# Kernel tuning notes

Measured on AMD Instinct MI355X. Metric: run time of the kernel, lower is better.

Reference implementation:

```python
import jax, jax.numpy as jnp
import numpy as np

N_PATCHES = 14
HIDDEN_D = 768
LN_EPS = 1e-5


def positional_embeddings(seq_len, d):
    # sin(i / 10000^(j/d)) for even j, cos(i / 10000^((j-1)/d)) for odd j
    i = jnp.arange(seq_len, dtype=jnp.float32)[:, None]
    j = jnp.arange(d, dtype=jnp.float32)[None, :]
    exponent = (jnp.floor(j / 2.0) * 2.0) / d
    angle = i / jnp.power(10000.0, exponent)
    return jnp.where(jnp.arange(d)[None, :] % 2 == 0, jnp.sin(angle), jnp.cos(angle))


def patchify(images, n_patches):
    # images: [B, C, H, W] -> patches: [B, n_patches^2, C*ph*pw]
    # flatten order per torch patch.flatten(): (C, ph, pw)
    B, C, H, W = images.shape
    ph, pw = H // n_patches, W // n_patches
    x = images.reshape(B, C, n_patches, ph, n_patches, pw)
    x = x.transpose(0, 2, 4, 1, 3, 5)  # [B, ny, nx, C, ph, pw]
    return x.reshape(B, n_patches * n_patches, C * ph * pw)


def setup_inputs() -> dict:
    key = jax.random.key(0)
    k_img, k_w, k_b, k_cls = jax.random.split(key, 4)
    B, C, H, W = 128, 3, 224, 224
    lin_in = (H // N_PATCHES) * (W // N_PATCHES) * C  # 768
    bound = 1.0 / np.sqrt(lin_in)
    return {
        "images": jax.random.normal(k_img, (B, C, H, W), dtype=jnp.float32),
        "W": jax.random.uniform(k_w, (HIDDEN_D, lin_in), jnp.float32, -bound, bound),
        "b": jax.random.uniform(k_b, (HIDDEN_D,), jnp.float32, -bound, bound),
        "class_token": jax.random.uniform(k_cls, (1, HIDDEN_D), jnp.float32),
        "gamma": jnp.ones((HIDDEN_D,), jnp.float32),
        "beta": jnp.zeros((HIDDEN_D,), jnp.float32),
    }


def reference(images, W, b, class_token, gamma, beta):
    B = images.shape[0]
    patches = patchify(images, N_PATCHES)                # [B, P^2, lin_in]
    tokens = jnp.einsum("bpi,di->bpd", patches, W) + b   # [B, P^2, D]
    cls = jnp.broadcast_to(class_token[None, :, :], (B, 1, HIDDEN_D))
    tokens = jnp.concatenate([cls, tokens], axis=1)      # [B, P^2+1, D]
    pos = positional_embeddings(N_PATCHES ** 2 + 1, HIDDEN_D)
    out = tokens + pos[None, :, :]
    mean = out.mean(axis=-1, keepdims=True)
    var = out.var(axis=-1, keepdims=True)
    out = (out - mean) / jnp.sqrt(var + LN_EPS)
    return out * gamma + beta
```

## Files before the change

### kernel.cpp

```cpp
#include <hip/hip_runtime.h>


#define IMG_B 128
#define IMG_C 3
#define IMG_HW 224
#define NPATCH 14
#define DTOK 768
#define NTOK 197
#define MROWS 25088

typedef __attribute__((ext_vector_type(4))) float f32x4;
typedef __attribute__((ext_vector_type(8))) short bf16x8;
typedef __attribute__((ext_vector_type(4))) short bf16x4;

__device__ __forceinline__ unsigned short f2b(float f) {
  union { float f; unsigned u; } v; v.f = f;
  unsigned u = v.u;
  return (unsigned short)((u + 0x7fffu + ((u >> 16) & 1u)) >> 16);
}


__global__ void conv_w(const float* __restrict__ W, unsigned short* __restrict__ Wb) {
  int i = blockIdx.x * 256 + threadIdx.x;
  if (i < DTOK * DTOK) Wb[i] = f2b(W[i]);
}

__global__ void make_bpos(const float* __restrict__ bias, const float* __restrict__ cls,
                          float* __restrict__ bpos) {
  int i = blockIdx.x * 256 + threadIdx.x;
  if (i >= NTOK * DTOK) return;
  int t = i / DTOK, d = i - (i / DTOK) * DTOK;
  float expo = (float)(d & ~1) * (1.0f / (float)DTOK);
  float angle = (float)t * exp2f(-expo * 13.287712379549449f);
  float pv = (d & 1) ? cosf(angle) : sinf(angle);
  bpos[i] = pv + ((t == 0) ? cls[d] : bias[d]);
}

__global__ __launch_bounds__(256) void cls_kernel(const float* __restrict__ bpos,
                                                  const float* __restrict__ gamma,
                                                  const float* __restrict__ beta,
                                                  float* __restrict__ out) {
  __shared__ float sred[8];
  const int tid = threadIdx.x;
  float v0 = bpos[tid], v1 = bpos[tid + 256], v2 = bpos[tid + 512];
  float s1 = v0 + v1 + v2;
  float s2 = v0 * v0 + v1 * v1 + v2 * v2;
  #pragma unroll
  for (int off = 32; off >= 1; off >>= 1) {
    s1 += __shfl_xor(s1, off, 64);
    s2 += __shfl_xor(s2, off, 64);
  }
  if ((tid & 63) == 0) { sred[(tid >> 6) * 2] = s1; sred[(tid >> 6) * 2 + 1] = s2; }
  __syncthreads();
  float S1 = sred[0] + sred[2] + sred[4] + sred[6];
  float S2 = sred[1] + sred[3] + sred[5] + sred[7];
  float mean = S1 * (1.0f / 768.0f);
  float rstd = rsqrtf(S2 * (1.0f / 768.0f) - mean * mean + 1e-5f);
  float o0 = (v0 - mean) * rstd * gamma[tid] + beta[tid];
  float o1 = (v1 - mean) * rstd * gamma[tid + 256] + beta[tid + 256];
  float o2 = (v2 - mean) * rstd * gamma[tid + 512] + beta[tid + 512];
  for (int b = 0; b < IMG_B; ++b) {
    float* op = out + (size_t)b * NTOK * DTOK;
    op[tid] = o0; op[tid + 256] = o1; op[tid + 512] = o2;
  }
}


__global__ __launch_bounds__(512) void vit_main(
    const float* __restrict__ images, const unsigned short* __restrict__ Wb,
    const float* __restrict__ bpos, const float* __restrict__ gamma,
    const float* __restrict__ beta, float* __restrict__ out) {
  __shared__ unsigned short Alds[64][40];
  __shared__ float red[8][64][2];
  __shared__ float rowstat[64][2];

  const int tid = threadIdx.x;
  const int wid = tid >> 6;
  const int lane = tid & 63;
  const int l15 = lane & 15;
  const int g = lane >> 4;
  const int blk = blockIdx.x;
  const int cbase = wid * 96;

  const int srow = tid >> 3;
  const int kq = tid & 7;
  const int kloc = kq * 4;
  const int sm = blk * 64 + srow;
  const int sb = sm / 196;
  const int sp = sm - sb * 196;
  const int spy = sp / 14, spx = sp - (sp / 14) * 14;
  const float* sbase =
      images + (size_t)sb * (IMG_C * IMG_HW * IMG_HW) + (spy * 16) * IMG_HW + spx * 16;

  f32x4 acc[4][6];
  #pragma unroll
  for (int mf = 0; mf < 4; ++mf)
    #pragma unroll
    for (int nf = 0; nf < 6; ++nf)
      acc[mf][nf] = (f32x4)(0.0f);

  for (int it = 0; it < 24; ++it) {
    const int k0 = it * 32;
    const int k = k0 + kloc;
    const int c = k >> 8;
    const int ph = (k & 255) >> 4;
    const int pw = k & 15;
    const float4 vv = *(const float4*)(sbase + c * (IMG_HW * IMG_HW) + ph * IMG_HW + pw);
    bf16x4 h;
    h[0] = (short)f2b(vv.x); h[1] = (short)f2b(vv.y);
    h[2] = (short)f2b(vv.z); h[3] = (short)f2b(vv.w);

    __syncthreads();
    *(bf16x4*)&Alds[srow][kloc] = h;
    __syncthreads();

    bf16x8 afr[4];
    #pragma unroll
    for (int mf = 0; mf < 4; ++mf)
      afr[mf] = *(const bf16x8*)&Alds[mf * 16 + l15][g * 8];

    bf16x8 bfr[6];
    #pragma unroll
    for (int nf = 0; nf < 6; ++nf)
      bfr[nf] = *(const bf16x8*)(Wb + (size_t)(cbase + nf * 16 + l15) * DTOK + k0 + g * 8);

    #pragma unroll
    for (int mf = 0; mf < 4; ++mf)
      #pragma unroll
      for (int nf = 0; nf < 6; ++nf)
        acc[mf][nf] =
            __builtin_amdgcn_mfma_f32_16x16x32_bf16(afr[mf], bfr[nf], acc[mf][nf], 0, 0, 0);
  }

  float s1[16], s2[16];
  #pragma unroll
  for (int mf = 0; mf < 4; ++mf) {
    #pragma unroll
    for (int r = 0; r < 4; ++r) {
      const int rl = mf * 16 + g * 4 + r;
      const int m = blk * 64 + rl;
      const int trow = 1 + (m % 196);
      const float* bp = bpos + (size_t)trow * DTOK + cbase + l15;
      float a1 = 0.f, a2 = 0.f;
      #pragma unroll
      for (int nf = 0; nf < 6; ++nf) {
        float val = acc[mf][nf][r] + bp[nf * 16];
        acc[mf][nf][r] = val;
        a1 += val; a2 += val * val;
      }
      s1[mf * 4 + r] = a1; s2[mf * 4 + r] = a2;
    }
  }
  #pragma unroll
  for (int off = 8; off >= 1; off >>= 1) {
    #pragma unroll
    for (int i = 0; i < 16; ++i) {
      s1[i] += __shfl_xor(s1[i], off, 64);
      s2[i] += __shfl_xor(s2[i], off, 64);
    }
  }
  if (l15 == 0) {
    #pragma unroll
    for (int mf = 0; mf < 4; ++mf)
      #pragma unroll
      for (int r = 0; r < 4; ++r) {
        const int rl = mf * 16 + g * 4 + r;
        red[wid][rl][0] = s1[mf * 4 + r];
        red[wid][rl][1] = s2[mf * 4 + r];
      }
  }
  __syncthreads();
  if (tid < 64) {
    float S1 = 0.f, S2 = 0.f;
    #pragma unroll
    for (int w = 0; w < 8; ++w) { S1 += red[w][tid][0]; S2 += red[w][tid][1]; }
    float mean = S1 * (1.0f / 768.0f);
    float var = S2 * (1.0f / 768.0f) - mean * mean;
    rowstat[tid][0] = mean;
    rowstat[tid][1] = rsqrtf(var + 1e-5f);
  }
  __syncthreads();

  float gm[6], bt[6];
  #pragma unroll
  for (int nf = 0; nf < 6; ++nf) {
    gm[nf] = gamma[cbase + nf * 16 + l15];
    bt[nf] = beta[cbase + nf * 16 + l15];
  }
  #pragma unroll
  for (int mf = 0; mf < 4; ++mf) {
    #pragma unroll
    for (int r = 0; r < 4; ++r) {
      const int rl = mf * 16 + g * 4 + r;
      const int m = blk * 64 + rl;
      const int bb = m / 196;
      const int orow = bb * 197 + 1 + (m - bb * 196);
      const float mean = rowstat[rl][0], rstd = rowstat[rl][1];
      float* op = out + (size_t)orow * DTOK + cbase + l15;
      #pragma unroll
      for (int nf = 0; nf < 6; ++nf)
        op[nf * 16] = (acc[mf][nf][r] - mean) * rstd * gm[nf] + bt[nf];
    }
  }
}

extern "C" void kernel_launch(void* const* d_in, const int* in_sizes, int n_in,
                              void* d_out, int out_size, void* d_ws, size_t ws_size,
                              hipStream_t stream) {
  const float* images = (const float*)d_in[0];
  const float* W      = (const float*)d_in[1];
  const float* bias   = (const float*)d_in[2];
  const float* cls    = (const float*)d_in[3];
  const float* gamma  = (const float*)d_in[4];
  const float* beta   = (const float*)d_in[5];
  float* out = (float*)d_out;

  unsigned short* Wb = (unsigned short*)d_ws;
  float* bpos = (float*)((char*)d_ws + (size_t)DTOK * DTOK * 2);

  conv_w<<<(DTOK * DTOK + 255) / 256, 256, 0, stream>>>(W, Wb);
  make_bpos<<<(NTOK * DTOK + 255) / 256, 256, 0, stream>>>(bias, cls, bpos);
  cls_kernel<<<1, 256, 0, stream>>>(bpos, gamma, beta, out);
  vit_main<<<MROWS / 64, 512, 0, stream>>>(images, Wb, bpos, gamma, beta, out);
}
```

Before: 133.5 us.

## Double-buffer A tile in LDS and prefetch image and weight fragments

The GEMM main loop now uses two LDS buffers for the activation tile. Image loads are prefetched two iterations ahead and bf16 weight fragments one iteration ahead into registers, so global-load latency overlaps the MFMA work. The two __syncthreads per iteration become one manual lgkmcnt wait plus s_barrier, and address math is precomputed into fixed strides. This raises register pressure, since two weight fragment sets and two image vectors are kept live, which may lower occupancy.

```diff
diff --git a/kernel.cpp b/kernel.cpp
--- a/kernel.cpp
+++ b/kernel.cpp
@@ -4,7 +4,6 @@
 #define IMG_B 128
 #define IMG_C 3
 #define IMG_HW 224
-#define NPATCH 14
 #define DTOK 768
 #define NTOK 197
 #define MROWS 25088
@@ -70,7 +69,7 @@
     const float* __restrict__ images, const unsigned short* __restrict__ Wb,
     const float* __restrict__ bpos, const float* __restrict__ gamma,
     const float* __restrict__ beta, float* __restrict__ out) {
-  __shared__ unsigned short Alds[64][40];
+  __shared__ unsigned short Alds[2][64][40];
   __shared__ float red[8][64][2];
   __shared__ float rowstat[64][2];
 
@@ -89,8 +88,9 @@
   const int sb = sm / 196;
   const int sp = sm - sb * 196;
   const int spy = sp / 14, spx = sp - (sp / 14) * 14;
-  const float* sbase =
-      images + (size_t)sb * (IMG_C * IMG_HW * IMG_HW) + (spy * 16) * IMG_HW + spx * 16;
+  const float* sbase2 = images + (size_t)sb * (IMG_C * IMG_HW * IMG_HW) +
+                        (spy * 16) * IMG_HW + spx * 16 + (kq >> 2) * IMG_HW + (kq & 3) * 4;
+  const unsigned short* wbase = Wb + (size_t)(cbase + l15) * DTOK + g * 8;
 
   f32x4 acc[4][6];
   #pragma unroll
@@ -99,38 +99,65 @@
     for (int nf = 0; nf < 6; ++nf)
       acc[mf][nf] = (f32x4)(0.0f);
 
-  for (int it = 0; it < 24; ++it) {
-    const int k0 = it * 32;
-    const int k = k0 + kloc;
-    const int c = k >> 8;
-    const int ph = (k & 255) >> 4;
-    const int pw = k & 15;
-    const float4 vv = *(const float4*)(sbase + c * (IMG_HW * IMG_HW) + ph * IMG_HW + pw);
+  float4 rimg[2];
+  bf16x8 bfr[2][6];
+
+  rimg[0] = *(const float4*)(sbase2);
+  rimg[1] = *(const float4*)(sbase2 + 448);
+  #pragma unroll
+  for (int nf = 0; nf < 6; ++nf)
+    bfr[0][nf] = *(const bf16x8*)(wbase + nf * 12288);
+  {
+    float4 rv = rimg[0];
     bf16x4 h;
-    h[0] = (short)f2b(vv.x); h[1] = (short)f2b(vv.y);
-    h[2] = (short)f2b(vv.z); h[3] = (short)f2b(vv.w);
-
-    __syncthreads();
-    *(bf16x4*)&Alds[srow][kloc] = h;
-    __syncthreads();
-
-    bf16x8 afr[4];
-    #pragma unroll
-    for (int mf = 0; mf < 4; ++mf)
-      afr[mf] = *(const bf16x8*)&Alds[mf * 16 + l15][g * 8];
-
-    bf16x8 bfr[6];
-    #pragma unroll
-    for (int nf = 0; nf < 6; ++nf)
-      bfr[nf] = *(const bf16x8*)(Wb + (size_t)(cbase + nf * 16 + l15) * DTOK + k0 + g * 8);
-
-    #pragma unroll
-    for (int mf = 0; mf < 4; ++mf)
-      #pragma unroll
-      for (int nf = 0; nf < 6; ++nf)
-        acc[mf][nf] =
-            __builtin_amdgcn_mfma_f32_16x16x32_bf16(afr[mf], bfr[nf], acc[mf][nf], 0, 0, 0);
-  }
+    h[0] = (short)f2b(rv.x); h[1] = (short)f2b(rv.y);
+    h[2] = (short)f2b(rv.z); h[3] = (short)f2b(rv.w);
+    *(bf16x4*)&Alds[0][srow][kloc] = h;
+  }
+  asm volatile("s_waitcnt lgkmcnt(0)" ::: "memory");
+  __builtin_amdgcn_s_barrier();
+  asm volatile("" ::: "memory");
+
+#define K_BODY(CUR, IT)                                                            \
+  {                                                                                \
+    if ((IT) + 2 < 24)                                                             \
+      rimg[CUR] = *(const float4*)(sbase2 + (((IT) + 2) >> 3) * 50176 +            \
+                                   (((IT) + 2) & 7) * 448);                        \
+    if ((IT) + 1 < 24) {                                                           \
+      _Pragma("unroll")                                                            \
+      for (int nf = 0; nf < 6; ++nf)                                               \
+        bfr[(CUR) ^ 1][nf] =                                                       \
+            *(const bf16x8*)(wbase + nf * 12288 + ((IT) + 1) * 32);                \
+    }                                                                              \
+    bf16x8 afr[4];                                                                 \
+    _Pragma("unroll")                                                              \
+    for (int mf = 0; mf < 4; ++mf)                                                 \
+      afr[mf] = *(const bf16x8*)&Alds[CUR][mf * 16 + l15][g * 8];                  \
+    _Pragma("unroll")                                                              \
+    for (int nf = 0; nf < 6; ++nf) {                                               \
+      _Pragma("unroll")                                                            \
+      for (int mf = 0; mf < 4; ++mf)                                               \
+        acc[mf][nf] = __builtin_amdgcn_mfma_f32_16x16x32_bf16(                     \
+            afr[mf], bfr[CUR][nf], acc[mf][nf], 0, 0, 0);                          \
+    }                                                                              \
+    if ((IT) + 1 < 24) {                                                           \
+      float4 rv = rimg[(CUR) ^ 1];                                                 \
+      bf16x4 h;                                                                    \
+      h[0] = (short)f2b(rv.x); h[1] = (short)f2b(rv.y);                            \
+      h[2] = (short)f2b(rv.z); h[3] = (short)f2b(rv.w);                            \
+      *(bf16x4*)&Alds[(CUR) ^ 1][srow][kloc] = h;                                  \
+    }                                                                              \
+    asm volatile("s_waitcnt lgkmcnt(0)" ::: "memory");                             \
+    __builtin_amdgcn_s_barrier();                                                  \
+    asm volatile("" ::: "memory");                                                 \
+  }
+
+  for (int jt = 0; jt < 12; ++jt) {
+    const int it = jt * 2;
+    K_BODY(0, it)
+    K_BODY(1, it + 1)
+  }
+#undef K_BODY
 
   float s1[16], s2[16];
   #pragma unroll
```

Measured after the change: 107.1 us. 1.25x faster.

## Load A fragments directly from global, drop LDS staging and barriers

Applied to the files above, without the earlier changes.

The main GEMM kernel now uses 32-row tiles with 4 waves, each covering 192 output columns. Each lane loads its own A fragment straight from the image (two float4 loads) and converts it to bf16 in registers, which removes the LDS staging buffer and the two barriers per k-step. The k-loop is fully unrolled and B pointers are precomputed. In exchange, each 32-row block re-reads the weight matrix for only 32 rows, which doubles total W traffic, and the larger accumulator array raises register pressure.

```diff
diff --git a/kernel.cpp b/kernel.cpp
--- a/kernel.cpp
+++ b/kernel.cpp
@@ -1,17 +1,16 @@
 #include <hip/hip_runtime.h>
+#include <hip/hip_bf16.h>
 
 
 #define IMG_B 128
 #define IMG_C 3
 #define IMG_HW 224
-#define NPATCH 14
 #define DTOK 768
 #define NTOK 197
 #define MROWS 25088
 
 typedef __attribute__((ext_vector_type(4))) float f32x4;
 typedef __attribute__((ext_vector_type(8))) short bf16x8;
-typedef __attribute__((ext_vector_type(4))) short bf16x4;
 
 __device__ __forceinline__ unsigned short f2b(float f) {
   union { float f; unsigned u; } v; v.f = f;
@@ -66,84 +65,83 @@
 }
 
 
-__global__ __launch_bounds__(512) void vit_main(
+__global__ __launch_bounds__(256, 2) void vit_main(
     const float* __restrict__ images, const unsigned short* __restrict__ Wb,
     const float* __restrict__ bpos, const float* __restrict__ gamma,
     const float* __restrict__ beta, float* __restrict__ out) {
-  __shared__ unsigned short Alds[64][40];
-  __shared__ float red[8][64][2];
-  __shared__ float rowstat[64][2];
+  __shared__ float red[4][32][2];
+  __shared__ float rowstat[32][2];
 
   const int tid = threadIdx.x;
-  const int wid = tid >> 6;
+  const int wq = tid >> 6;
   const int lane = tid & 63;
   const int l15 = lane & 15;
   const int g = lane >> 4;
   const int blk = blockIdx.x;
-  const int cbase = wid * 96;
-
-  const int srow = tid >> 3;
-  const int kq = tid & 7;
-  const int kloc = kq * 4;
-  const int sm = blk * 64 + srow;
-  const int sb = sm / 196;
-  const int sp = sm - sb * 196;
-  const int spy = sp / 14, spx = sp - (sp / 14) * 14;
-  const float* sbase =
-      images + (size_t)sb * (IMG_C * IMG_HW * IMG_HW) + (spy * 16) * IMG_HW + spx * 16;
-
-  f32x4 acc[4][6];
-  #pragma unroll
-  for (int mf = 0; mf < 4; ++mf)
-    #pragma unroll
-    for (int nf = 0; nf < 6; ++nf)
+  const int cbase = wq * 192;
+
+  const float* abase[2];
+  #pragma unroll
+  for (int mf = 0; mf < 2; ++mf) {
+    const int m = blk * 32 + mf * 16 + l15;
+    const int sb = m / 196;
+    const int sp = m - sb * 196;
+    const int spy = sp / 14, spx = sp - (sp / 14) * 14;
+    abase[mf] = images + (size_t)sb * (IMG_C * IMG_HW * IMG_HW) +
+                (spy * 16) * IMG_HW + spx * 16 + (g & 1) * 8;
+  }
+  const int gb = g >> 1;
+
+  const unsigned short* bbase[12];
+  #pragma unroll
+  for (int nf = 0; nf < 12; ++nf)
+    bbase[nf] = Wb + (size_t)(cbase + nf * 16 + l15) * DTOK + g * 8;
+
+  f32x4 acc[2][12];
+  #pragma unroll
+  for (int mf = 0; mf < 2; ++mf)
+    #pragma unroll
+    for (int nf = 0; nf < 12; ++nf)
       acc[mf][nf] = (f32x4)(0.0f);
 
+  #pragma unroll
   for (int it = 0; it < 24; ++it) {
-    const int k0 = it * 32;
-    const int k = k0 + kloc;
-    const int c = k >> 8;
-    const int ph = (k & 255) >> 4;
-    const int pw = k & 15;
-    const float4 vv = *(const float4*)(sbase + c * (IMG_HW * IMG_HW) + ph * IMG_HW + pw);
-    bf16x4 h;
-    h[0] = (short)f2b(vv.x); h[1] = (short)f2b(vv.y);
-    h[2] = (short)f2b(vv.z); h[3] = (short)f2b(vv.w);
-
-    __syncthreads();
-    *(bf16x4*)&Alds[srow][kloc] = h;
-    __syncthreads();
-
-    bf16x8 afr[4];
-    #pragma unroll
-    for (int mf = 0; mf < 4; ++mf)
-      afr[mf] = *(const bf16x8*)&Alds[mf * 16 + l15][g * 8];
-
-    bf16x8 bfr[6];
-    #pragma unroll
-    for (int nf = 0; nf < 6; ++nf)
-      bfr[nf] = *(const bf16x8*)(Wb + (size_t)(cbase + nf * 16 + l15) * DTOK + k0 + g * 8);
-
-    #pragma unroll
-    for (int mf = 0; mf < 4; ++mf)
-      #pragma unroll
-      for (int nf = 0; nf < 6; ++nf)
-        acc[mf][nf] =
-            __builtin_amdgcn_mfma_f32_16x16x32_bf16(afr[mf], bfr[nf], acc[mf][nf], 0, 0, 0);
-  }
-
-  float s1[16], s2[16];
-  #pragma unroll
-  for (int mf = 0; mf < 4; ++mf) {
+    const int idx = it * 2 + gb;
+    const int aoff = (idx >> 4) * (IMG_HW * IMG_HW) + (idx & 15) * IMG_HW;
+
+    bf16x8 afr[2];
+    #pragma unroll
+    for (int mf = 0; mf < 2; ++mf) {
+      const float4 v0 = *(const float4*)(abase[mf] + aoff);
+      const float4 v1 = *(const float4*)(abase[mf] + aoff + 4);
+      union { __hip_bfloat162 h2[4]; bf16x8 v; } u;
+      u.h2[0] = __float22bfloat162_rn(make_float2(v0.x, v0.y));
+      u.h2[1] = __float22bfloat162_rn(make_float2(v0.z, v0.w));
+      u.h2[2] = __float22bfloat162_rn(make_float2(v1.x, v1.y));
+      u.h2[3] = __float22bfloat162_rn(make_float2(v1.z, v1.w));
+      afr[mf] = u.v;
+    }
+
+    #pragma unroll
+    for (int nf = 0; nf < 12; ++nf) {
+      const bf16x8 bf = *(const bf16x8*)(bbase[nf] + it * 32);
+      acc[0][nf] = __builtin_amdgcn_mfma_f32_16x16x32_bf16(afr[0], bf, acc[0][nf], 0, 0, 0);
+      acc[1][nf] = __builtin_amdgcn_mfma_f32_16x16x32_bf16(afr[1], bf, acc[1][nf], 0, 0, 0);
+    }
+  }
+
+  float s1[8], s2[8];
+  #pragma unroll
+  for (int mf = 0; mf < 2; ++mf) {
     #pragma unroll
     for (int r = 0; r < 4; ++r) {
       const int rl = mf * 16 + g * 4 + r;
-      const int m = blk * 64 + rl;
+      const int m = blk * 32 + rl;
       const int trow = 1 + (m % 196);
       const float* bp = bpos + (size_t)trow * DTOK + cbase + l15;
       float a1 = 0.f, a2 = 0.f;
       #pragma unroll
-      for (int nf = 0; nf < 6; ++nf) {
+      for (int nf = 0; nf < 12; ++nf) {
         float val = acc[mf][nf][r] + bp[nf * 16];
         acc[mf][nf][r] = val;
         a1 += val; a2 += val * val;
@@ -154,26 +152,25 @@
   #pragma unroll
   for (int off = 8; off >= 1; off >>= 1) {
     #pragma unroll
-    for (int i = 0; i < 16; ++i) {
+    for (int i = 0; i < 8; ++i) {
       s1[i] += __shfl_xor(s1[i], off, 64);
       s2[i] += __shfl_xor(s2[i], off, 64);
     }
   }
   if (l15 == 0) {
     #pragma unroll
-    for (int mf = 0; mf < 4; ++mf)
+    for (int mf = 0; mf < 2; ++mf)
       #pragma unroll
       for (int r = 0; r < 4; ++r) {
         const int rl = mf * 16 + g * 4 + r;
-        red[wid][rl][0] = s1[mf * 4 + r];
-        red[wid][rl][1] = s2[mf * 4 + r];
+        red[wq][rl][0] = s1[mf * 4 + r];
+        red[wq][rl][1] = s2[mf * 4 + r];
       }
   }
   __syncthreads();
-  if (tid < 64) {
-    float S1 = 0.f, S2 = 0.f;
-    #pragma unroll
-    for (int w = 0; w < 8; ++w) { S1 += red[w][tid][0]; S2 += red[w][tid][1]; }
+  if (tid < 32) {
+    float S1 = red[0][tid][0] + red[1][tid][0] + red[2][tid][0] + red[3][tid][0];
+    float S2 = red[0][tid][1] + red[1][tid][1] + red[2][tid][1] + red[3][tid][1];
     float mean = S1 * (1.0f / 768.0f);
     float var = S2 * (1.0f / 768.0f) - mean * mean;
     rowstat[tid][0] = mean;
@@ -181,24 +178,24 @@
   }
   __syncthreads();
 
-  float gm[6], bt[6];
-  #pragma unroll
-  for (int nf = 0; nf < 6; ++nf) {
+  float gm[12], bt[12];
+  #pragma unroll
+  for (int nf = 0; nf < 12; ++nf) {
     gm[nf] = gamma[cbase + nf * 16 + l15];
     bt[nf] = beta[cbase + nf * 16 + l15];
   }
   #pragma unroll
-  for (int mf = 0; mf < 4; ++mf) {
+  for (int mf = 0; mf < 2; ++mf) {
     #pragma unroll
     for (int r = 0; r < 4; ++r) {
       const int rl = mf * 16 + g * 4 + r;
-      const int m = blk * 64 + rl;
+      const int m = blk * 32 + rl;
       const int bb = m / 196;
       const int orow = bb * 197 + 1 + (m - bb * 196);
       const float mean = rowstat[rl][0], rstd = rowstat[rl][1];
       float* op = out + (size_t)orow * DTOK + cbase + l15;
       #pragma unroll
-      for (int nf = 0; nf < 6; ++nf)
+      for (int nf = 0; nf < 12; ++nf)
         op[nf * 16] = (acc[mf][nf][r] - mean) * rstd * gm[nf] + bt[nf];
     }
   }
@@ -221,5 +218,5 @@
   conv_w<<<(DTOK * DTOK + 255) / 256, 256, 0, stream>>>(W, Wb);
   make_bpos<<<(NTOK * DTOK + 255) / 256, 256, 0, stream>>>(bias, cls, bpos);
   cls_kernel<<<1, 256, 0, stream>>>(bpos, gamma, beta, out);
-  vit_main<<<MROWS / 64, 512, 0, stream>>>(images, Wb, bpos, gamma, beta, out);
-}
+  vit_main<<<MROWS / 32, 256, 0, stream>>>(images, Wb, bpos, gamma, beta, out);
+}
```

After: 197.2 us. 1.48x slower.

## Double-buffer A and W tiles in LDS with async global-to-LDS loads

Applied to the files above, without the earlier changes.

The main GEMM loop now stages both the image patch tile and the bf16 weight tile in double-buffered shared memory. Weights are fetched with global_load_lds directly into an XOR-swizzled layout, and the next iteration's loads are issued before the current MFMAs, so only one barrier is needed per k-step. This aims to hide global memory latency and avoid bank conflicts on the weight reads, which previously came straight from global memory into registers. The cost is about 100KB of LDS per block, which limits occupancy to one block per CU, and added index arithmetic.

```diff
diff --git a/kernel.cpp b/kernel.cpp
--- a/kernel.cpp
+++ b/kernel.cpp
@@ -1,10 +1,10 @@
 #include <hip/hip_runtime.h>
+#include <hip/hip_bf16.h>
 
 
 #define IMG_B 128
 #define IMG_C 3
 #define IMG_HW 224
-#define NPATCH 14
 #define DTOK 768
 #define NTOK 197
 #define MROWS 25088
@@ -17,6 +17,12 @@
   union { float f; unsigned u; } v; v.f = f;
   unsigned u = v.u;
   return (unsigned short)((u + 0x7fffu + ((u >> 16) & 1u)) >> 16);
+}
+
+__device__ __forceinline__ void glds16(const void* g, void* l) {
+  __builtin_amdgcn_global_load_lds(
+      (const __attribute__((address_space(1))) unsigned int*)g,
+      (__attribute__((address_space(3))) unsigned int*)l, 16, 0, 0);
 }
 
 
@@ -70,7 +76,8 @@
     const float* __restrict__ images, const unsigned short* __restrict__ Wb,
     const float* __restrict__ bpos, const float* __restrict__ gamma,
     const float* __restrict__ beta, float* __restrict__ out) {
-  __shared__ unsigned short Alds[64][40];
+  __shared__ unsigned short Bl[2][24576];
+  __shared__ unsigned short Al[2][2048];
   __shared__ float red[8][64][2];
   __shared__ float rowstat[64][2];
 
@@ -84,13 +91,28 @@
 
   const int srow = tid >> 3;
   const int kq = tid & 7;
-  const int kloc = kq * 4;
   const int sm = blk * 64 + srow;
   const int sb = sm / 196;
   const int sp = sm - sb * 196;
   const int spy = sp / 14, spx = sp - (sp / 14) * 14;
-  const float* sbase =
-      images + (size_t)sb * (IMG_C * IMG_HW * IMG_HW) + (spy * 16) * IMG_HW + spx * 16;
+  const float* abase = images + (size_t)sb * (IMG_C * IMG_HW * IMG_HW) +
+                       (spy * 16) * IMG_HW + spx * 16 + (kq & 3) * 4;
+  const int bq = kq >> 2;
+  const int aw_idx = (srow * 4 + ((kq >> 1) ^ ((srow >> 1) & 3))) * 8 + (kq & 1) * 4;
+
+  int boff[6];
+  #pragma unroll
+  for (int j = 0; j < 6; ++j) {
+    const int d = j * 512 + tid;
+    const int r = d >> 2;
+    const int q = (d & 3) ^ ((r >> 1) & 3);
+    boff[j] = r * DTOK + q * 8;
+  }
+  const int bldsbase = wid * 512;
+
+  const int sA = g ^ ((l15 >> 1) & 3);
+  const int ard = l15 * 32 + sA * 8;
+  const int brd = cbase * 32 + l15 * 32 + sA * 8;
 
   f32x4 acc[4][6];
   #pragma unroll
@@ -99,37 +121,51 @@
     for (int nf = 0; nf < 6; ++nf)
       acc[mf][nf] = (f32x4)(0.0f);
 
-  for (int it = 0; it < 24; ++it) {
-    const int k0 = it * 32;
-    const int k = k0 + kloc;
-    const int c = k >> 8;
-    const int ph = (k & 255) >> 4;
-    const int pw = k & 15;
-    const float4 vv = *(const float4*)(sbase + c * (IMG_HW * IMG_HW) + ph * IMG_HW + pw);
-    bf16x4 h;
-    h[0] = (short)f2b(vv.x); h[1] = (short)f2b(vv.y);
-    h[2] = (short)f2b(vv.z); h[3] = (short)f2b(vv.w);
-
+  {
+    const int v = bq;
+    const float4 av = *(const float4*)(abase + (v >> 4) * 50176 + (v & 15) * 224);
+    #pragma unroll
+    for (int j = 0; j < 6; ++j)
+      glds16(Wb + boff[j], &Bl[0][bldsbase + j * 4096]);
+    union { __hip_bfloat162 h2[2]; bf16x4 v4; } u;
+    u.h2[0] = __float22bfloat162_rn(make_float2(av.x, av.y));
+    u.h2[1] = __float22bfloat162_rn(make_float2(av.z, av.w));
+    *(bf16x4*)&Al[0][aw_idx] = u.v4;
     __syncthreads();
-    *(bf16x4*)&Alds[srow][kloc] = h;
+  }
+
+  for (int k = 0; k < 24; ++k) {
+    const int cur = k & 1, nxt = cur ^ 1;
+    float4 av;
+    if (k < 23) {
+      const int v = (k + 1) * 2 + bq;
+      av = *(const float4*)(abase + (v >> 4) * 50176 + (v & 15) * 224);
+      #pragma unroll
+      for (int j = 0; j < 6; ++j)
+        glds16(Wb + boff[j] + (k + 1) * 32, &Bl[nxt][bldsbase + j * 4096]);
+    }
+
+    bf16x8 afr[4];
+    #pragma unroll
+    for (int mf = 0; mf < 4; ++mf)
+      afr[mf] = *(const bf16x8*)&Al[cur][ard + mf * 512];
+
+    #pragma unroll
+    for (int nf = 0; nf < 6; ++nf) {
+      const bf16x8 bf = *(const bf16x8*)&Bl[cur][brd + nf * 512];
+      #pragma unroll
+      for (int mf = 0; mf < 4; ++mf)
+        acc[mf][nf] =
+            __builtin_amdgcn_mfma_f32_16x16x32_bf16(afr[mf], bf, acc[mf][nf], 0, 0, 0);
+    }
+
+    if (k < 23) {
+      union { __hip_bfloat162 h2[2]; bf16x4 v4; } u;
+      u.h2[0] = __float22bfloat162_rn(make_float2(av.x, av.y));
+      u.h2[1] = __float22bfloat162_rn(make_float2(av.z, av.w));
+      *(bf16x4*)&Al[nxt][aw_idx] = u.v4;
+    }
     __syncthreads();
-
-    bf16x8 afr[4];
-    #pragma unroll
-    for (int mf = 0; mf < 4; ++mf)
-      afr[mf] = *(const bf16x8*)&Alds[mf * 16 + l15][g * 8];
-
-    bf16x8 bfr[6];
-    #pragma unroll
-    for (int nf = 0; nf < 6; ++nf)
-      bfr[nf] = *(const bf16x8*)(Wb + (size_t)(cbase + nf * 16 + l15) * DTOK + k0 + g * 8);
-
-    #pragma unroll
-    for (int mf = 0; mf < 4; ++mf)
-      #pragma unroll
-      for (int nf = 0; nf < 6; ++nf)
-        acc[mf][nf] =
-            __builtin_amdgcn_mfma_f32_16x16x32_bf16(afr[mf], bfr[nf], acc[mf][nf], 0, 0, 0);
   }
 
   float s1[16], s2[16];
```

Result: faster. 110.3 us (-17.4%).
